# Kernel optimization log

Hardware: AMD Instinct MI355X
Metric: run time of the kernel (lower is better)

The kernel has to match this reference:

```python
import jax, jax.numpy as jnp
import numpy as np

N = 100000       # nodes
E = 3200000      # edges (avg degree 32)
NFEAT = 128
NHID = 128
NCLASS = 64


def setup_inputs() -> dict:
    key = jax.random.key(0)
    ks = jax.random.split(key, 8)
    x = jax.random.normal(ks[0], (N, NFEAT), dtype=jnp.float32)
    edge_index = jax.random.randint(ks[1], (2, E), 0, N, dtype=jnp.int64)
    s1 = 1.0 / np.sqrt(NFEAT)
    s2 = 1.0 / np.sqrt(NHID)
    return {
        "x": x,
        "edge_index": edge_index,
        "W1_self": jax.random.normal(ks[2], (NFEAT, NHID), dtype=jnp.float32) * s1,
        "W1_neigh": jax.random.normal(ks[3], (NFEAT, NHID), dtype=jnp.float32) * s1,
        "b1": jnp.zeros((NHID,), dtype=jnp.float32),
        "W2_self": jax.random.normal(ks[4], (NHID, NCLASS), dtype=jnp.float32) * s2,
        "W2_neigh": jax.random.normal(ks[5], (NHID, NCLASS), dtype=jnp.float32) * s2,
        "b2": jnp.zeros((NCLASS,), dtype=jnp.float32),
    }


def _sage_conv(h, src, dst, inv_deg, W_self, W_neigh, b):
    # gather source features, scatter-add to destinations, mean-normalize
    agg = jax.ops.segment_sum(h[src], dst, num_segments=N)  # [N, F]
    mean = agg * inv_deg[:, None]
    return h @ W_self + mean @ W_neigh + b


def reference(x, edge_index, W1_self, W1_neigh, b1, W2_self, W2_neigh, b2):
    src, dst = edge_index[0], edge_index[1]
    deg = jax.ops.segment_sum(jnp.ones((E,), dtype=x.dtype), dst, num_segments=N)
    inv_deg = 1.0 / jnp.maximum(deg, 1.0)
    h = _sage_conv(x, src, dst, inv_deg, W1_self, W1_neigh, b1)
    h = jax.nn.relu(h)
    # F.dropout with training=False is identity (inference mode)
    out = _sage_conv(h, src, dst, inv_deg, W2_self, W2_neigh, b2)
    return out
```

## Files before the change

kernel.cpp:

```cpp
#include <hip/hip_runtime.h>

#define NNODES 100000
#define NEDGES 3200000
#define NBKT 196
#define NTILES2 1563
#define NGB 1563

typedef unsigned int uint;
typedef unsigned short ushort;
typedef unsigned char uchar;
typedef __attribute__((ext_vector_type(8))) short short8;
typedef __attribute__((ext_vector_type(4))) float f32x4;
typedef __attribute__((ext_vector_type(2))) float f32x2;

__device__ inline ushort bf16_rne(float f) {
    uint u = __float_as_uint(f);
    return (ushort)((u + 0x7FFFu + ((u >> 16) & 1u)) >> 16);
}
__device__ inline uint pack_bf2(float a, float b) {
    return (uint)bf16_rne(a) | ((uint)bf16_rne(b) << 16);
}
__device__ inline float2 unpack_bf2(uint v) {
    float2 r;
    r.x = __uint_as_float(v << 16);
    r.y = __uint_as_float(v & 0xFFFF0000u);
    return r;
}

__device__ inline uchar f32_to_fp8(float f) {
    uint u = __float_as_uint(f);
    uint s = (u >> 24) & 0x80u;
    uint e = (u >> 23) & 0xFFu;
    if (e < 121u) return (uchar)s;
    uint m = u & 0x7FFFFFu;
    uint r = (m + 0x7FFFFu + ((m >> 20) & 1u)) >> 20;
    uint em = ((e - 120u) << 3) + r;
    return (uchar)(s | em);
}
__device__ inline float fp8_dec(uint b) {
    uint s = (b & 0x80u) << 24;
    uint em = b & 0x7Fu;
    float v = __uint_as_float(s | ((em + 960u) << 20));
    return em ? v : 0.0f;
}
__device__ inline float2 fp8_lo2(uint pk) {
#if __has_builtin(__builtin_amdgcn_cvt_pk_f32_fp8)
    f32x2 r = __builtin_amdgcn_cvt_pk_f32_fp8((int)pk, false);
    return make_float2(r[0], r[1]);
#else
    return make_float2(fp8_dec(pk & 0xFFu), fp8_dec((pk >> 8) & 0xFFu));
#endif
}
__device__ inline float2 fp8_hi2(uint pk) {
#if __has_builtin(__builtin_amdgcn_cvt_pk_f32_fp8)
    f32x2 r = __builtin_amdgcn_cvt_pk_f32_fp8((int)pk, true);
    return make_float2(r[0], r[1]);
#else
    return make_float2(fp8_dec((pk >> 16) & 0xFFu), fp8_dec(pk >> 24));
#endif
}

__global__ __launch_bounds__(256) void histprep_kernel(
    const int* __restrict__ dst, int* __restrict__ bhist,
    const float* __restrict__ W1s, const float* __restrict__ W1n,
    const float* __restrict__ W2s, const float* __restrict__ W2n,
    ushort* __restrict__ wt) {
    if (blockIdx.x >= 512) {
        const int id = (blockIdx.x - 512) * 256 + threadIdx.x;
        const int m = id >> 14;
        const int r = id & 16383;
        const int c = r >> 7;
        const int k = r & 127;
        float v;
        if (m == 0) v = W1s[k * 128 + c];
        else if (m == 1) v = W1n[k * 128 + c];
        else v = (c < 64) ? W2s[k * 64 + c] : W2n[k * 64 + (c - 64)];
        wt[id] = bf16_rne(v);
        return;
    }
    __shared__ int lh[NBKT];
    for (int i = threadIdx.x; i < NBKT; i += 256) lh[i] = 0;
    __syncthreads();
    const int n4 = NEDGES / 4;
    for (int i = blockIdx.x * 256 + threadIdx.x; i < n4; i += 512 * 256) {
        const int4 d = ((const int4*)dst)[i];
        atomicAdd(&lh[d.x >> 9], 1);
        atomicAdd(&lh[d.y >> 9], 1);
        atomicAdd(&lh[d.z >> 9], 1);
        atomicAdd(&lh[d.w >> 9], 1);
    }
    __syncthreads();
    for (int i = threadIdx.x; i < NBKT; i += 256)
        if (lh[i]) atomicAdd(&bhist[i], lh[i]);
}

__global__ __launch_bounds__(256) void scan_bkt(const int* __restrict__ bhist,
                                                int* __restrict__ boff,
                                                int* __restrict__ gcur,
                                                int* __restrict__ rs) {
    __shared__ int s[256];
    const int tid = threadIdx.x;
    const int v = (tid < NBKT) ? bhist[tid] : 0;
    s[tid] = v;
    __syncthreads();
    for (int ofs = 1; ofs < 256; ofs <<= 1) {
        int t = (tid >= ofs) ? s[tid - ofs] : 0;
        __syncthreads();
        s[tid] += t;
        __syncthreads();
    }
    const int excl = s[tid] - v;
    if (tid < NBKT) {
        boff[tid] = excl;
        gcur[tid] = excl;
    }
    if (tid == NBKT - 1) {
        boff[NBKT] = s[tid];
        rs[NNODES] = NEDGES;
    }
}

__global__ __launch_bounds__(256) void megaA_kernel(
    const float* __restrict__ x, const ushort* __restrict__ wt,
    const float* __restrict__ b1, ushort* __restrict__ hbf,
    uchar* __restrict__ xnf8, const int* __restrict__ src,
    const int* __restrict__ dst, int* __restrict__ gcur,
    uint* __restrict__ pairbuf) {
    __shared__ uint4 sWq[4096];
    const int bid = blockIdx.x;
    const int tid = threadIdx.x;

    if (bid & 1) {
        int* ib = (int*)sWq;
        int* lhist = ib;
        int* lofs = ib + 256;
        int* gbl = ib + 512;
        int* lcur = ib + 768;
        const int t = bid >> 1;
        const int ebase = t * 2048;
        const int n = min(2048, NEDGES - ebase);
        const int nv4 = n >> 2;
        lhist[tid] = 0;
        lcur[tid] = 0;
        __syncthreads();
        int4 sv[2], dv[2];
#pragma unroll
        for (int u = 0; u < 2; ++u) {
            const int i4 = tid + 256 * u;
            if (i4 < nv4) {
                sv[u] = ((const int4*)(src + ebase))[i4];
                dv[u] = ((const int4*)(dst + ebase))[i4];
                atomicAdd(&lhist[dv[u].x >> 9], 1);
                atomicAdd(&lhist[dv[u].y >> 9], 1);
                atomicAdd(&lhist[dv[u].z >> 9], 1);
                atomicAdd(&lhist[dv[u].w >> 9], 1);
            }
        }
        __syncthreads();
        const int v = lhist[tid];
        lofs[tid] = v;
        __syncthreads();
        for (int ofs = 1; ofs < 256; ofs <<= 1) {
            int tv = (tid >= ofs) ? lofs[tid - ofs] : 0;
            __syncthreads();
            lofs[tid] += tv;
            __syncthreads();
        }
        if (tid < NBKT && v > 0) gbl[tid] = atomicAdd(&gcur[tid], v);
        __syncthreads();
#pragma unroll
        for (int u = 0; u < 2; ++u) {
            const int i4 = tid + 256 * u;
            if (i4 < nv4) {
                const int ss[4] = {sv[u].x, sv[u].y, sv[u].z, sv[u].w};
                const int dd[4] = {dv[u].x, dv[u].y, dv[u].z, dv[u].w};
#pragma unroll
                for (int j = 0; j < 4; ++j) {
                    const int b = dd[j] >> 9;
                    const int p = atomicAdd(&lcur[b], 1);
                    pairbuf[gbl[b] + p] =
                        ((uint)ss[j] << 9) | ((uint)dd[j] & 511u);
                }
            }
        }
        return;
    }

    const int g = bid >> 1;
#pragma unroll
    for (int i = 0; i < 16; ++i) {
        const int cid = tid + 256 * i;
        const int kc = cid & 15;
        const int c = (cid >> 4) & 127;
        const int wsel = cid >> 11;
        sWq[wsel * 2048 + c * 16 + (kc ^ (c & 15))] = *(const uint4*)&wt[cid * 8];
    }
    const int w = tid >> 6;
    const int l = tid & 63;
    const int lg = l >> 4;
    const int lr = l & 15;
    const int rowbase = g * 64;
    const int arow = min(rowbase + w * 16 + lr, NNODES - 1);
    const float* xrow = x + (size_t)arow * 128;
    short8 ahi[4], alo[4];
#pragma unroll
    for (int ks = 0; ks < 4; ++ks) {
        const float4 va = *(const float4*)&xrow[ks * 32 + lg * 8];
        const float4 vb = *(const float4*)&xrow[ks * 32 + lg * 8 + 4];
        const float vv[8] = {va.x, va.y, va.z, va.w, vb.x, vb.y, vb.z, vb.w};
        short8 h8, l8;
#pragma unroll
        for (int j = 0; j < 8; ++j) {
            const ushort hu = bf16_rne(vv[j]);
            h8[j] = (short)hu;
            l8[j] = (short)bf16_rne(vv[j] - __uint_as_float((uint)hu << 16));
        }
        ahi[ks] = h8;
        alo[ks] = l8;
    }
    __syncthreads();

#pragma unroll
    for (int wsel = 0; wsel < 2; ++wsel) {
#pragma unroll
        for (int ct = 0; ct < 8; ++ct) {
            f32x4 acc;
            if (wsel == 0) {
                const float bv = b1[ct * 16 + lr];
                acc = (f32x4){bv, bv, bv, bv};
            } else {
                acc = (f32x4){0.0f, 0.0f, 0.0f, 0.0f};
            }
            const int cbase = wsel * 2048 + (ct * 16 + lr) * 16;
#pragma unroll
            for (int ks = 0; ks < 4; ++ks) {
                const short8 bf =
                    *(const short8*)&sWq[cbase + ((4 * ks + lg) ^ lr)];
                acc = __builtin_amdgcn_mfma_f32_16x16x32_bf16(ahi[ks], bf, acc, 0, 0, 0);
                acc = __builtin_amdgcn_mfma_f32_16x16x32_bf16(alo[ks], bf, acc, 0, 0, 0);
            }
#pragma unroll
            for (int r_ = 0; r_ < 4; ++r_) {
                const int orow = rowbase + w * 16 + lg * 4 + r_;
                if (orow < NNODES) {
                    if (wsel == 0)
                        hbf[(size_t)orow * 128 + ct * 16 + lr] = bf16_rne(acc[r_]);
                    else
                        xnf8[(size_t)orow * 128 + ct * 16 + lr] = f32_to_fp8(acc[r_]);
                }
            }
        }
    }
}

__global__ __launch_bounds__(256) void bucket_kernel(const uint* __restrict__ pairbuf,
                                                     const int* __restrict__ boff,
                                                     int* __restrict__ rs,
                                                     float* __restrict__ invd,
                                                     int* __restrict__ ebuf) {
    __shared__ int ndeg[512];
    __shared__ int nofs[512];
    __shared__ int lcur[512];
    __shared__ int sps[256];
    const int b = blockIdx.x;
    const int tid = threadIdx.x;
    const int nb = b << 9;
    const int ln = min(512, NNODES - nb);
    const int base = boff[b];
    const int cnt = boff[b + 1] - base;
    for (int i = tid; i < 512; i += 256) {
        ndeg[i] = 0;
        lcur[i] = 0;
    }
    __syncthreads();
    for (int i = tid; i < cnt; i += 256) {
        atomicAdd(&ndeg[pairbuf[base + i] & 511u], 1);
    }
    __syncthreads();
    for (int nidx = tid; nidx < ln; nidx += 256)
        invd[nb + nidx] = 1.0f / fmaxf((float)ndeg[nidx], 1.0f);
    const int a0 = ndeg[2 * tid];
    const int a1 = ndeg[2 * tid + 1];
    sps[tid] = a0 + a1;
    __syncthreads();
    for (int ofs = 1; ofs < 256; ofs <<= 1) {
        int t = (tid >= ofs) ? sps[tid - ofs] : 0;
        __syncthreads();
        sps[tid] += t;
        __syncthreads();
    }
    const int excl = sps[tid] - (a0 + a1);
    nofs[2 * tid] = excl;
    nofs[2 * tid + 1] = excl + a0;
    __syncthreads();
    for (int nidx = tid; nidx < ln; nidx += 256) rs[nb + nidx] = base + nofs[nidx];
    for (int i = tid; i < cnt; i += 256) {
        const uint e = pairbuf[base + i];
        const int nn = (int)(e & 511u);
        const int p = atomicAdd(&lcur[nn], 1);
        ebuf[base + nofs[nn] + p] = (int)(e >> 9);
    }
}

__global__ __launch_bounds__(256) void gemm2_dual_kernel(
    const ushort* __restrict__ hbf, const ushort* __restrict__ wt2,
    const float* __restrict__ b2, float* __restrict__ out,
    uchar* __restrict__ hnf8) {
    __shared__ uint4 sWq[2048];
    const int tid = threadIdx.x;
#pragma unroll
    for (int i = 0; i < 8; ++i) {
        const int cid = tid + 256 * i;
        const int kc = cid & 15;
        const int c = cid >> 4;
        sWq[c * 16 + (kc ^ (c & 15))] = *(const uint4*)&wt2[cid * 8];
    }
    const int w = tid >> 6;
    const int l = tid & 63;
    const int lg = l >> 4;
    const int lr = l & 15;
    const int rowbase = blockIdx.x * 64;
    const int arow = min(rowbase + w * 16 + lr, NNODES - 1);
    const ushort* hrow = hbf + (size_t)arow * 128;
    short8 a[4];
#pragma unroll
    for (int ks = 0; ks < 4; ++ks) a[ks] = *(const short8*)&hrow[ks * 32 + lg * 8];
    __syncthreads();

#pragma unroll
    for (int ct = 0; ct < 8; ++ct) {
        f32x4 acc;
        if (ct < 4) {
            const float bv = b2[ct * 16 + lr];
            acc = (f32x4){bv, bv, bv, bv};
        } else {
            acc = (f32x4){0.0f, 0.0f, 0.0f, 0.0f};
        }
        const int cbase = (ct * 16 + lr) * 16;
#pragma unroll
        for (int ks = 0; ks < 4; ++ks) {
            const short8 bf = *(const short8*)&sWq[cbase + ((4 * ks + lg) ^ lr)];
            acc = __builtin_amdgcn_mfma_f32_16x16x32_bf16(a[ks], bf, acc, 0, 0, 0);
        }
#pragma unroll
        for (int r_ = 0; r_ < 4; ++r_) {
            const int orow = rowbase + w * 16 + lg * 4 + r_;
            if (orow < NNODES) {
                if (ct < 4)
                    out[(size_t)orow * 64 + ct * 16 + lr] = acc[r_];
                else
                    hnf8[(size_t)orow * 64 + (ct - 4) * 16 + lr] = f32_to_fp8(acc[r_]);
            }
        }
    }
}

__global__ __launch_bounds__(256) void agg1_kernel(const int* __restrict__ rs,
                                                   const int* __restrict__ ebuf,
                                                   const float* __restrict__ invd,
                                                   const uchar* __restrict__ xnf8,
                                                   ushort* __restrict__ hbf) {
    const int node = blockIdx.x * 8 + (threadIdx.x >> 5);
    if (node >= NNODES) return;
    const int lane = threadIdx.x & 31;
    const int beg = rs[node];
    const int end = rs[node + 1];
    const uint* fp = (const uint*)xnf8 + lane;
    float a0 = 0.0f, a1 = 0.0f, a2 = 0.0f, a3 = 0.0f;
    int i = beg;
    for (; i + 3 < end; i += 4) {
#pragma unroll
        for (int u = 0; u < 4; ++u) {
            const uint pk = fp[(size_t)ebuf[i + u] * 32];
            const float2 lo = fp8_lo2(pk);
            const float2 hi = fp8_hi2(pk);
            a0 += lo.x; a1 += lo.y; a2 += hi.x; a3 += hi.y;
        }
    }
    for (; i < end; ++i) {
        const uint pk = fp[(size_t)ebuf[i] * 32];
        const float2 lo = fp8_lo2(pk);
        const float2 hi = fp8_hi2(pk);
        a0 += lo.x; a1 += lo.y; a2 += hi.x; a3 += hi.y;
    }
    const float w = invd[node];
    uint* hp = (uint*)hbf + (size_t)node * 64 + lane * 2;
    uint2 hv = *(uint2*)hp;
    float2 h0 = unpack_bf2(hv.x);
    float2 h1 = unpack_bf2(hv.y);
    h0.x = fmaxf(fmaf(w, a0, h0.x), 0.0f);
    h0.y = fmaxf(fmaf(w, a1, h0.y), 0.0f);
    h1.x = fmaxf(fmaf(w, a2, h1.x), 0.0f);
    h1.y = fmaxf(fmaf(w, a3, h1.y), 0.0f);
    hv.x = pack_bf2(h0.x, h0.y);
    hv.y = pack_bf2(h1.x, h1.y);
    *(uint2*)hp = hv;
}

__global__ __launch_bounds__(256) void agg2_kernel(const int* __restrict__ rs,
                                                   const int* __restrict__ ebuf,
                                                   const float* __restrict__ invd,
                                                   const uchar* __restrict__ hnf8,
                                                   float* __restrict__ out) {
    const int node = blockIdx.x * 8 + (threadIdx.x >> 5);
    if (node >= NNODES) return;
    const int lane = threadIdx.x & 31;
    const int beg = rs[node];
    const int end = rs[node + 1];
    const ushort* fp = (const ushort*)hnf8 + lane;
    float a0 = 0.0f, a1 = 0.0f;
    int i = beg;
    for (; i + 3 < end; i += 4) {
#pragma unroll
        for (int u = 0; u < 4; ++u) {
            const uint pk = (uint)fp[(size_t)ebuf[i + u] * 32];
            const float2 v = fp8_lo2(pk);
            a0 += v.x; a1 += v.y;
        }
    }
    for (; i < end; ++i) {
        const uint pk = (uint)fp[(size_t)ebuf[i] * 32];
        const float2 v = fp8_lo2(pk);
        a0 += v.x; a1 += v.y;
    }
    const float w = invd[node];
    float2* op = (float2*)&out[(size_t)node * 64 + lane * 2];
    float2 ov = *op;
    ov.x = fmaf(w, a0, ov.x);
    ov.y = fmaf(w, a1, ov.y);
    *op = ov;
}

extern "C" void kernel_launch(void* const* d_in, const int* in_sizes, int n_in,
                              void* d_out, int out_size, void* d_ws, size_t ws_size,
                              hipStream_t stream) {
    const float* x   = (const float*)d_in[0];
    const int*   ei  = (const int*)d_in[1];
    const float* W1s = (const float*)d_in[2];
    const float* W1n = (const float*)d_in[3];
    const float* b1  = (const float*)d_in[4];
    const float* W2s = (const float*)d_in[5];
    const float* W2n = (const float*)d_in[6];
    const float* b2  = (const float*)d_in[7];
    float* out = (float*)d_out;

    const int* src = ei;
    const int* dst = ei + NEDGES;

    int* w = (int*)d_ws;
    int*    bhist   = w;
    int*    boff    = w + 256;
    int*    gcur    = w + 512;
    int*    rs      = w + 768;
    float*  invd    = (float*)(w + 100864);
    int*    ebuf    = w + 200864;
    uint*   pairbuf = (uint*)(w + 3400864);
    uchar*  xnf8    = (uchar*)(w + 6600864);
    ushort* hbf     = (ushort*)(w + 9800864);
    ushort* wtbuf   = (ushort*)(w + 16200864);
    uchar*  hnf8    = xnf8;

    hipMemsetAsync(bhist, 0, 256 * sizeof(int), stream);
    histprep_kernel<<<704, 256, 0, stream>>>(dst, bhist, W1s, W1n, W2s, W2n, wtbuf);
    scan_bkt<<<1, 256, 0, stream>>>(bhist, boff, gcur, rs);

    megaA_kernel<<<2 * NTILES2, 256, 0, stream>>>(x, wtbuf, b1, hbf, xnf8, src, dst,
                                                  gcur, pairbuf);
    bucket_kernel<<<NBKT, 256, 0, stream>>>(pairbuf, boff, rs, invd, ebuf);

    agg1_kernel<<<NNODES / 8, 256, 0, stream>>>(rs, ebuf, invd, xnf8, hbf);

    gemm2_dual_kernel<<<NGB, 256, 0, stream>>>(hbf, wtbuf + 32768, b2, out, hnf8);
    agg2_kernel<<<NNODES / 8, 256, 0, stream>>>(rs, ebuf, invd, hnf8, out);
}
```

Baseline: 273.4 us.

## Read GEMM weight fragments directly from global memory instead of staging in LDS

The two MFMA GEMM kernels no longer copy the bf16 weight matrix into swizzled shared memory. Each lane now loads its B fragment straight from global memory, which relies on L2/L1 caching since the weights are tiny. This removes the per-block LDS fill and barrier and shrinks megaA's LDS from 64KB to 4KB, allowing more resident blocks. The cost is repeated global/L1 loads inside the MFMA loop, with partial unrolling to limit register pressure. The histogram kernel also now uses 128 blocks instead of 512.

```diff
diff --git a/kernel.cpp b/kernel.cpp
--- a/kernel.cpp
+++ b/kernel.cpp
@@ -65,8 +65,8 @@
     const float* __restrict__ W1s, const float* __restrict__ W1n,
     const float* __restrict__ W2s, const float* __restrict__ W2n,
     ushort* __restrict__ wt) {
-    if (blockIdx.x >= 512) {
-        const int id = (blockIdx.x - 512) * 256 + threadIdx.x;
+    if (blockIdx.x >= 128) {
+        const int id = (blockIdx.x - 128) * 256 + threadIdx.x;
         const int m = id >> 14;
         const int r = id & 16383;
         const int c = r >> 7;
@@ -82,7 +82,7 @@
     for (int i = threadIdx.x; i < NBKT; i += 256) lh[i] = 0;
     __syncthreads();
     const int n4 = NEDGES / 4;
-    for (int i = blockIdx.x * 256 + threadIdx.x; i < n4; i += 512 * 256) {
+    for (int i = blockIdx.x * 256 + threadIdx.x; i < n4; i += 128 * 256) {
         const int4 d = ((const int4*)dst)[i];
         atomicAdd(&lh[d.x >> 9], 1);
         atomicAdd(&lh[d.y >> 9], 1);
@@ -126,16 +126,15 @@
     uchar* __restrict__ xnf8, const int* __restrict__ src,
     const int* __restrict__ dst, int* __restrict__ gcur,
     uint* __restrict__ pairbuf) {
-    __shared__ uint4 sWq[4096];
+    __shared__ int smem[1024];
     const int bid = blockIdx.x;
     const int tid = threadIdx.x;
 
     if (bid & 1) {
-        int* ib = (int*)sWq;
-        int* lhist = ib;
-        int* lofs = ib + 256;
-        int* gbl = ib + 512;
-        int* lcur = ib + 768;
+        int* lhist = smem;
+        int* lofs = smem + 256;
+        int* gbl = smem + 512;
+        int* lcur = smem + 768;
         const int t = bid >> 1;
         const int ebase = t * 2048;
         const int n = min(2048, NEDGES - ebase);
@@ -187,14 +186,6 @@
     }
 
     const int g = bid >> 1;
-#pragma unroll
-    for (int i = 0; i < 16; ++i) {
-        const int cid = tid + 256 * i;
-        const int kc = cid & 15;
-        const int c = (cid >> 4) & 127;
-        const int wsel = cid >> 11;
-        sWq[wsel * 2048 + c * 16 + (kc ^ (c & 15))] = *(const uint4*)&wt[cid * 8];
-    }
     const int w = tid >> 6;
     const int l = tid & 63;
     const int lg = l >> 4;
@@ -218,11 +209,10 @@
         ahi[ks] = h8;
         alo[ks] = l8;
     }
-    __syncthreads();
 
 #pragma unroll
     for (int wsel = 0; wsel < 2; ++wsel) {
-#pragma unroll
+#pragma unroll 4
         for (int ct = 0; ct < 8; ++ct) {
             f32x4 acc;
             if (wsel == 0) {
@@ -231,11 +221,10 @@
             } else {
                 acc = (f32x4){0.0f, 0.0f, 0.0f, 0.0f};
             }
-            const int cbase = wsel * 2048 + (ct * 16 + lr) * 16;
+            const ushort* wcol = wt + (size_t)((wsel << 7) + ct * 16 + lr) * 128;
 #pragma unroll
             for (int ks = 0; ks < 4; ++ks) {
-                const short8 bf =
-                    *(const short8*)&sWq[cbase + ((4 * ks + lg) ^ lr)];
+                const short8 bf = *(const short8*)&wcol[(ks * 4 + lg) * 8];
                 acc = __builtin_amdgcn_mfma_f32_16x16x32_bf16(ahi[ks], bf, acc, 0, 0, 0);
                 acc = __builtin_amdgcn_mfma_f32_16x16x32_bf16(alo[ks], bf, acc, 0, 0, 0);
             }
@@ -306,15 +295,7 @@
     const ushort* __restrict__ hbf, const ushort* __restrict__ wt2,
     const float* __restrict__ b2, float* __restrict__ out,
     uchar* __restrict__ hnf8) {
-    __shared__ uint4 sWq[2048];
     const int tid = threadIdx.x;
-#pragma unroll
-    for (int i = 0; i < 8; ++i) {
-        const int cid = tid + 256 * i;
-        const int kc = cid & 15;
-        const int c = cid >> 4;
-        sWq[c * 16 + (kc ^ (c & 15))] = *(const uint4*)&wt2[cid * 8];
-    }
     const int w = tid >> 6;
     const int l = tid & 63;
     const int lg = l >> 4;
@@ -325,9 +306,8 @@
     short8 a[4];
 #pragma unroll
     for (int ks = 0; ks < 4; ++ks) a[ks] = *(const short8*)&hrow[ks * 32 + lg * 8];
-    __syncthreads();
-
-#pragma unroll
+
+#pragma unroll 4
     for (int ct = 0; ct < 8; ++ct) {
         f32x4 acc;
         if (ct < 4) {
@@ -336,10 +316,10 @@
         } else {
             acc = (f32x4){0.0f, 0.0f, 0.0f, 0.0f};
         }
-        const int cbase = (ct * 16 + lr) * 16;
+        const ushort* wcol = wt2 + (size_t)(ct * 16 + lr) * 128;
 #pragma unroll
         for (int ks = 0; ks < 4; ++ks) {
-            const short8 bf = *(const short8*)&sWq[cbase + ((4 * ks + lg) ^ lr)];
+            const short8 bf = *(const short8*)&wcol[(ks * 4 + lg) * 8];
             acc = __builtin_amdgcn_mfma_f32_16x16x32_bf16(a[ks], bf, acc, 0, 0, 0);
         }
 #pragma unroll
@@ -461,7 +441,7 @@
     uchar*  hnf8    = xnf8;
 
     hipMemsetAsync(bhist, 0, 256 * sizeof(int), stream);
-    histprep_kernel<<<704, 256, 0, stream>>>(dst, bhist, W1s, W1n, W2s, W2n, wtbuf);
+    histprep_kernel<<<320, 256, 0, stream>>>(dst, bhist, W1s, W1n, W2s, W2n, wtbuf);
     scan_bkt<<<1, 256, 0, stream>>>(bhist, boff, gcur, rs);
 
     megaA_kernel<<<2 * NTILES2, 256, 0, stream>>>(x, wtbuf, b1, hbf, xnf8, src, dst,
```

After: 344.0 us. 25.8% more time.
